# Performance work log

Hardware: AMD Instinct MI355X
Metric: run time of the kernel (lower is better)

The kernel has to match this reference:

```python
import jax, jax.numpy as jnp
import numpy as np

D_MODEL = 1024
IDX_DIM = 64
SEQ = 4096
D_STATE = 64
EXPAND = 1
HEADDIM = 32
D_CONV = 4
D_INNER = EXPAND * D_MODEL
NHEADS = D_INNER // HEADDIM
CONV_DIM = D_INNER + 2 * D_STATE
D_IN_PROJ = 2 * D_INNER + 2 * D_STATE + NHEADS  # z, xBC, dt


def setup_inputs() -> dict:
    key = jax.random.key(0)
    ks = jax.random.split(key, 8)
    def rn(k, shape, scale=1.0):
        return jax.random.normal(k, shape, jnp.float32) * scale
    return {
        "x": rn(ks[0], (SEQ, D_MODEL)),
        "W_in": rn(ks[1], (D_IN_PROJ, D_MODEL), D_MODEL ** -0.5),
        "conv_w": rn(ks[2], (CONV_DIM, D_CONV), D_CONV ** -0.5),
        "conv_b": jnp.zeros((CONV_DIM,), jnp.float32),
        "dt_bias": rn(ks[3], (NHEADS,)),
        "A_log": jnp.log(jnp.arange(1, NHEADS + 1, dtype=jnp.float32)),
        "D": jnp.ones((NHEADS,), jnp.float32),
        "norm_w": jnp.ones((D_INNER,), jnp.float32),
        "W_out": rn(ks[4], (D_MODEL, D_INNER), D_INNER ** -0.5),
        "W_q": rn(ks[5], (IDX_DIM, D_MODEL), D_MODEL ** -0.5),
        "W_k": rn(ks[6], (IDX_DIM, D_MODEL), D_MODEL ** -0.5),
    }


def _silu(v):
    return v * jax.nn.sigmoid(v)


def _mamba2(x, W_in, conv_w, conv_b, dt_bias, A_log, Dp, norm_w, W_out):
    L = x.shape[0]
    zxbcdt = x @ W_in.T  # [L, D_IN_PROJ]
    z, xBC, dt = jnp.split(zxbcdt, [D_INNER, D_INNER + CONV_DIM], axis=-1)
    # depthwise causal conv1d, kernel D_CONV
    xc = jax.lax.conv_general_dilated(
        xBC.T[None],               # [1, C, L]
        conv_w[:, None, :],        # [C, 1, K]
        (1,), [(D_CONV - 1, 0)], feature_group_count=CONV_DIM)[0].T
    xBC = _silu(xc + conv_b)
    xs, B, C = jnp.split(xBC, [D_INNER, D_INNER + D_STATE], axis=-1)
    xs = xs.reshape(L, NHEADS, HEADDIM)
    dt = jax.nn.softplus(dt + dt_bias)   # [L, H]
    A = -jnp.exp(A_log)                  # [H]

    def step(h, inp):
        x_t, B_t, C_t, dt_t = inp        # [H,P], [N], [N], [H]
        dA = jnp.exp(dt_t * A)           # [H]
        h = h * dA[:, None, None] + (dt_t[:, None] * x_t)[:, :, None] * B_t[None, None, :]
        return h, jnp.einsum('hpn,n->hp', h, C_t)

    h0 = jnp.zeros((NHEADS, HEADDIM, D_STATE), x.dtype)
    _, ys = jax.lax.scan(step, h0, (xs, B, C, dt))  # ys: [L, H, P]
    y = ys + Dp[None, :, None] * xs
    y = y.reshape(L, D_INNER)
    y = y * _silu(z)                                 # gated RMSNorm
    y = y * jax.lax.rsqrt(jnp.mean(y * y, axis=-1, keepdims=True) + 1e-5) * norm_w
    return y @ W_out.T


def reference(x, W_in, conv_w, conv_b, dt_bias, A_log, D, norm_w, W_out, W_q, W_k):
    L = x.shape[0]
    x_mamba = _mamba2(x, W_in, conv_w, conv_b, dt_bias, A_log, D, norm_w, W_out)
    q = x_mamba @ W_q.T                  # [L, IDX_DIM]
    k = x @ W_k.T                        # [L, IDX_DIM]
    scores = jnp.einsum('ti,si->ts', q, k) * (IDX_DIM ** -0.5)
    mask = jnp.tril(jnp.ones((L, L), dtype=bool))
    return jnp.where(mask, scores, -jnp.inf)
```

## Files before the change

### kernel.cpp

```cpp
#include <hip/hip_runtime.h>
#include <math.h>

#define L_SEQ 4096
#define DMODEL 1024
#define DINNER 1024
#define DSTATE 64
#define NH 32
#define HD 32
#define CONVD 1152
#define DPROJ2 2272
#define KOFF 2208
#define QC 128
#define NC 32

#define NEG_FILL (-1e30f)

typedef __attribute__((ext_vector_type(8))) short short8;
typedef __attribute__((ext_vector_type(4))) float f32x4;
typedef unsigned short u16;

__device__ __forceinline__ u16 f2bf(float f) {
  unsigned int u = __float_as_uint(f);
  unsigned int r = (u + 0x7fffu + ((u >> 16) & 1u)) >> 16;
  return (u16)r;
}
__device__ __forceinline__ float bf2f(u16 b) {
  unsigned int u = ((unsigned int)b) << 16;
  return __uint_as_float(u);
}
__device__ __forceinline__ short8 pack8(float4 a, float4 b) {
  short8 v;
  v[0] = (short)f2bf(a.x); v[1] = (short)f2bf(a.y);
  v[2] = (short)f2bf(a.z); v[3] = (short)f2bf(a.w);
  v[4] = (short)f2bf(b.x); v[5] = (short)f2bf(b.y);
  v[6] = (short)f2bf(b.z); v[7] = (short)f2bf(b.w);
  return v;
}

__device__ __forceinline__ void g2l16(const void* g, void* l) {
  __builtin_amdgcn_global_load_lds(
      (const __attribute__((address_space(1))) unsigned int*)g,
      (__attribute__((address_space(3))) unsigned int*)l, 16, 0, 0);
}

#define CAST_N0 (L_SEQ * DMODEL / 8)
#define CAST_N1 (2208 * DMODEL / 8)
#define CAST_N2 (64 * DMODEL / 8)
#define CAST_TOTAL (CAST_N0 + CAST_N1 + 2 * CAST_N2)
__global__ __launch_bounds__(256) void cast_all_k(const float* __restrict__ x,
                                                  const float* __restrict__ W_in,
                                                  const float* __restrict__ W_k,
                                                  const float* __restrict__ W_q,
                                                  u16* __restrict__ x_bf,
                                                  u16* __restrict__ Wcat,
                                                  u16* __restrict__ Wq_bf) {
  int gid = blockIdx.x * 256 + threadIdx.x;
  const float* src;
  u16* dst;
  int i;
  if (gid < CAST_N0) { src = x; dst = x_bf; i = gid; }
  else if (gid < CAST_N0 + CAST_N1) { src = W_in; dst = Wcat; i = gid - CAST_N0; }
  else if (gid < CAST_N0 + CAST_N1 + CAST_N2) {
    src = W_k; dst = Wcat + (size_t)2208 * DMODEL; i = gid - CAST_N0 - CAST_N1;
  } else { src = W_q; dst = Wq_bf; i = gid - CAST_N0 - CAST_N1 - CAST_N2; }
  i *= 8;
  float4 f0 = *(const float4*)(src + i);
  float4 f1 = *(const float4*)(src + i + 4);
  *(short8*)(dst + i) = pack8(f0, f1);
}

__global__ __launch_bounds__(256) void transpose_cast_k(const float* __restrict__ in,
                                                        u16* __restrict__ out) {
  __shared__ float tile[64][65];
  int tx = threadIdx.x & 63, ty = threadIdx.x >> 6;
  int bx = blockIdx.x, by = blockIdx.y;
#pragma unroll
  for (int k = 0; k < 16; k++) {
    int r = ty + k * 4;
    tile[r][tx] = in[(size_t)(by * 64 + r) * 1024 + bx * 64 + tx];
  }
  __syncthreads();
#pragma unroll
  for (int k = 0; k < 16; k++) {
    int r = ty + k * 4;
    out[(size_t)(bx * 64 + r) * 1024 + by * 64 + tx] = f2bf(tile[tx][r]);
  }
}

__global__ __launch_bounds__(256) void wqo_k(const u16* __restrict__ Wq,
                                             const u16* __restrict__ WoutT,
                                             u16* __restrict__ Wqo) {
  const int tid = threadIdx.x;
  const int wave = tid >> 6, lane = tid & 63;
  const int l15 = lane & 15, quad = lane >> 4;
  const int j0 = blockIdx.x * 64;
  f32x4 acc[4] = {};
  for (int kk = 0; kk < 32; kk++) {
    short8 b = *(const short8*)(WoutT + (size_t)(j0 + wave * 16 + l15) * 1024 + kk * 32 + quad * 8);
#pragma unroll
    for (int mi = 0; mi < 4; mi++) {
      short8 a = *(const short8*)(Wq + (size_t)(mi * 16 + l15) * 1024 + kk * 32 + quad * 8);
      acc[mi] = __builtin_amdgcn_mfma_f32_16x16x32_bf16(a, b, acc[mi], 0, 0, 0);
    }
  }
#pragma unroll
  for (int mi = 0; mi < 4; mi++)
#pragma unroll
    for (int r = 0; r < 4; r++) {
      int i = mi * 16 + quad * 4 + r;
      Wqo[(size_t)i * 1024 + j0 + wave * 16 + l15] = f2bf(acc[mi][r]);
    }
}

__global__ __launch_bounds__(256) void gemm_n64(const u16* __restrict__ A,
                                                const u16* __restrict__ B,
                                                u16* __restrict__ Cbf,
                                                int M, int N, int K) {
  __shared__ u16 As[128 * 64];
  __shared__ u16 Bs[64 * 64];
  const int tid = threadIdx.x;
  const int wave = tid >> 6, lane = tid & 63;
  const int m0 = blockIdx.x * 128, n0 = blockIdx.y * 64;
  const int wm = (wave >> 1) * 64, wn = (wave & 1) * 32;
  const int l15 = lane & 15, quad = lane >> 4;

  const u16* aptr[4];
  const u16* bptr[2];
  char* ldsA[4];
  char* ldsB[2];
#pragma unroll
  for (int b = 0; b < 4; b++) {
    int ch = b * 256 + tid;
    int row = ch >> 3, q = (ch & 7) ^ (row & 7);
    aptr[b] = A + (size_t)(m0 + row) * K + q * 8;
    ldsA[b] = (char*)As + b * 4096 + wave * 1024;
  }
#pragma unroll
  for (int b = 0; b < 2; b++) {
    int ch = b * 256 + tid;
    int row = ch >> 3, q = (ch & 7) ^ (row & 7);
    int bn = min(n0 + row, N - 1);
    bptr[b] = B + (size_t)bn * K + q * 8;
    ldsB[b] = (char*)Bs + b * 4096 + wave * 1024;
  }

  int offA[2][4], offB[2][2];
#pragma unroll
  for (int kk = 0; kk < 2; kk++) {
#pragma unroll
    for (int i = 0; i < 4; i++) {
      int r = wm + i * 16 + l15;
      offA[kk][i] = r * 64 + ((kk * 4 + quad) ^ (r & 7)) * 8;
    }
#pragma unroll
    for (int j = 0; j < 2; j++) {
      int r = wn + j * 16 + l15;
      offB[kk][j] = r * 64 + ((kk * 4 + quad) ^ (r & 7)) * 8;
    }
  }

  f32x4 acc[4][2] = {};
  for (int k0 = 0; k0 < K; k0 += 64) {
#pragma unroll
    for (int b = 0; b < 4; b++) g2l16(aptr[b] + k0, ldsA[b]);
#pragma unroll
    for (int b = 0; b < 2; b++) g2l16(bptr[b] + k0, ldsB[b]);
    __builtin_amdgcn_s_waitcnt(0);
    __syncthreads();
#pragma unroll
    for (int kk = 0; kk < 2; kk++) {
      short8 af[4], bfr[2];
#pragma unroll
      for (int i = 0; i < 4; i++) af[i] = *(const short8*)(As + offA[kk][i]);
#pragma unroll
      for (int j = 0; j < 2; j++) bfr[j] = *(const short8*)(Bs + offB[kk][j]);
#pragma unroll
      for (int mi = 0; mi < 4; mi++)
#pragma unroll
        for (int ni = 0; ni < 2; ni++)
          acc[mi][ni] = __builtin_amdgcn_mfma_f32_16x16x32_bf16(af[mi], bfr[ni],
                                                                acc[mi][ni], 0, 0, 0);
    }
    __syncthreads();
  }
#pragma unroll
  for (int mi = 0; mi < 4; mi++)
#pragma unroll
    for (int r = 0; r < 4; r++) {
      int grow = m0 + wm + mi * 16 + quad * 4 + r;
#pragma unroll
      for (int ni = 0; ni < 2; ni++) {
        int gcol = n0 + wn + ni * 16 + l15;
        if (gcol < N) Cbf[(size_t)grow * N + gcol] = f2bf(acc[mi][ni][r]);
      }
    }
}

__global__ __launch_bounds__(256) void splitk64(const u16* __restrict__ A,
                                                const u16* __restrict__ B,
                                                float* __restrict__ P,
                                                int M, int K) {
  __shared__ u16 As[128 * 32];
  __shared__ u16 Bs[64 * 32];
  const int tid = threadIdx.x;
  const int wave = tid >> 6, lane = tid & 63;
  const int m0 = blockIdx.x * 128;
  const int ks = blockIdx.y;
  const int wm = (wave >> 1) * 64, wn = (wave & 1) * 32;
  const int l15 = lane & 15, quad = lane >> 4;

  const int c0 = tid, c1 = 256 + tid;
  const int r0 = c0 >> 2, q0 = (c0 & 3) ^ ((r0 >> 1) & 3);
  const int r1 = c1 >> 2, q1 = (c1 & 3) ^ ((r1 >> 1) & 3);
  const int rb = tid >> 2, qb = (tid & 3) ^ ((rb >> 1) & 3);
  const u16* a0 = A + (size_t)(m0 + r0) * K + q0 * 8;
  const u16* a1 = A + (size_t)(m0 + r1) * K + q1 * 8;
  const u16* bptr = B + (size_t)rb * K + qb * 8;
  char* ldsA0 = (char*)As + wave * 1024;
  char* ldsA1 = (char*)As + 4096 + wave * 1024;
  char* ldsB = (char*)Bs + wave * 1024;

  int offA[4], offB[2];
#pragma unroll
  for (int i = 0; i < 4; i++) {
    int ra = wm + i * 16 + l15;
    offA[i] = ra * 32 + (quad ^ ((ra >> 1) & 3)) * 8;
  }
#pragma unroll
  for (int j = 0; j < 2; j++) {
    int rr = wn + j * 16 + l15;
    offB[j] = rr * 32 + (quad ^ ((rr >> 1) & 3)) * 8;
  }

  f32x4 acc[4][2] = {};
  const int kbeg = ks * 128;
  for (int k0 = kbeg; k0 < kbeg + 128; k0 += 32) {
    g2l16(a0 + k0, ldsA0);
    g2l16(a1 + k0, ldsA1);
    g2l16(bptr + k0, ldsB);
    __builtin_amdgcn_s_waitcnt(0);
    __syncthreads();
    short8 af[4], bfr[2];
#pragma unroll
    for (int i = 0; i < 4; i++) af[i] = *(const short8*)(As + offA[i]);
#pragma unroll
    for (int j = 0; j < 2; j++) bfr[j] = *(const short8*)(Bs + offB[j]);
#pragma unroll
    for (int mi = 0; mi < 4; mi++)
#pragma unroll
      for (int ni = 0; ni < 2; ni++)
        acc[mi][ni] = __builtin_amdgcn_mfma_f32_16x16x32_bf16(af[mi], bfr[ni],
                                                              acc[mi][ni], 0, 0, 0);
    __syncthreads();
  }
  float* Pp = P + (size_t)ks * M * 64;
#pragma unroll
  for (int mi = 0; mi < 4; mi++)
#pragma unroll
    for (int r = 0; r < 4; r++) {
      int grow = m0 + wm + mi * 16 + quad * 4 + r;
#pragma unroll
      for (int ni = 0; ni < 2; ni++)
        Pp[(size_t)grow * 64 + wn + ni * 16 + l15] = acc[mi][ni][r];
    }
}

__global__ __launch_bounds__(256) void reduce8_k(const float* __restrict__ P,
                                                 u16* __restrict__ out, int n) {
  int i = blockIdx.x * 256 + threadIdx.x;
  if (i >= n) return;
  float s = 0.f;
#pragma unroll
  for (int ks = 0; ks < 8; ks++) s += P[(size_t)ks * n + i];
  out[i] = f2bf(s);
}

__global__ __launch_bounds__(256) void conv_silu_k(const u16* __restrict__ zx,
                                                   const float* __restrict__ cw,
                                                   const float* __restrict__ cb,
                                                   u16* __restrict__ xbc) {
  int gid = blockIdx.x * 256 + threadIdx.x;
  int t = gid / 144;
  int c0 = (gid - t * 144) * 8;
  float acc[8];
#pragma unroll
  for (int j = 0; j < 8; j++) acc[j] = cb[c0 + j];
  float wv[8][4];
#pragma unroll
  for (int j = 0; j < 8; j++) {
    float4 w4 = *(const float4*)(cw + (c0 + j) * 4);
    wv[j][0] = w4.x; wv[j][1] = w4.y; wv[j][2] = w4.z; wv[j][3] = w4.w;
  }
#pragma unroll
  for (int k = 0; k < 4; k++) {
    int s = t - 3 + k;
    if (s >= 0) {
      short8 v = *(const short8*)(zx + (size_t)s * DPROJ2 + DINNER + c0);
#pragma unroll
      for (int j = 0; j < 8; j++) acc[j] += bf2f((u16)v[j]) * wv[j][k];
    }
  }
  short8 o;
#pragma unroll
  for (int j = 0; j < 8; j++) o[j] = (short)f2bf(acc[j] / (1.f + expf(-acc[j])));
  *(short8*)(xbc + (size_t)t * CONVD + c0) = o;
}

__global__ void dtcum_k(const u16* __restrict__ zx,
                        const float* __restrict__ dt_bias,
                        const float* __restrict__ A_log,
                        float* __restrict__ dtsp,
                        float* __restrict__ aL) {
  int h = blockIdx.x & 31, c = blockIdx.x >> 5;
  int lane = threadIdx.x;
  float negA = -expf(A_log[h]);
  float bias = dt_bias[h];
  float carry = 0.f;
#pragma unroll
  for (int seg = 0; seg < 2; seg++) {
    int t = c * QC + seg * 64 + lane;
    float xv = bf2f(zx[(size_t)t * DPROJ2 + 2176 + h]) + bias;
    float sp = (xv > 20.f) ? xv : log1pf(expf(xv));
    dtsp[(size_t)t * 32 + h] = sp;
    float v = sp * negA;
#pragma unroll
    for (int off = 1; off < 64; off <<= 1) {
      float u = __shfl_up(v, off, 64);
      if (lane >= off) v += u;
    }
    aL[(size_t)t * 32 + h] = carry + v;
    carry += __shfl(v, 63, 64);
  }
}

__global__ __launch_bounds__(256) void chunk_state_mfma(const u16* __restrict__ xbc,
                                                        const float* __restrict__ dtsp,
                                                        const float* __restrict__ aL,
                                                        float* __restrict__ S) {
  int h = blockIdx.x & 31, c = blockIdx.x >> 5;
  int tid = threadIdx.x;
  __shared__ __align__(16) u16 sXs[32 * 136];
  __shared__ __align__(16) u16 sBT[64 * 136];
  __shared__ float scoef[QC];
  if (tid < QC) {
    float aend = aL[(size_t)(c * QC + QC - 1) * 32 + h];
    float a = aL[(size_t)(c * QC + tid) * 32 + h];
    scoef[tid] = expf(aend - a) * dtsp[(size_t)(c * QC + tid) * 32 + h];
  }
  __syncthreads();
  for (int j = tid; j < 32 * QC / 8; j += 256) {
    int s = j & 127, p0 = (j >> 7) * 8;
    short8 v = *(const short8*)(xbc + (size_t)(c * QC + s) * CONVD + h * HD + p0);
    float cf = scoef[s];
#pragma unroll
    for (int e = 0; e < 8; e++) sXs[(p0 + e) * 136 + s] = f2bf(cf * bf2f((u16)v[e]));
  }
  for (int j = tid; j < 64 * QC / 8; j += 256) {
    int s = j & 127, n0 = (j >> 7) * 8;
    short8 v = *(const short8*)(xbc + (size_t)(c * QC + s) * CONVD + DINNER + n0);
#pragma unroll
    for (int e = 0; e < 8; e++) sBT[(n0 + e) * 136 + s] = (u16)v[e];
  }
  __syncthreads();
  const int wave = tid >> 6, lane = tid & 63;
  const int l15 = lane & 15, quad = lane >> 4;
  f32x4 acc[2] = {};
#pragma unroll
  for (int kk = 0; kk < 4; kk++) {
    short8 b = *(const short8*)(sBT + (wave * 16 + l15) * 136 + kk * 32 + quad * 8);
#pragma unroll
    for (int i = 0; i < 2; i++) {
      short8 a = *(const short8*)(sXs + (i * 16 + l15) * 136 + kk * 32 + quad * 8);
      acc[i] = __builtin_amdgcn_mfma_f32_16x16x32_bf16(a, b, acc[i], 0, 0, 0);
    }
  }
  float* Sb = S + ((size_t)c * 32 + h) * 2048;
#pragma unroll
  for (int i = 0; i < 2; i++)
#pragma unroll
    for (int r = 0; r < 4; r++) {
      int p = i * 16 + quad * 4 + r;
      Sb[p * 64 + wave * 16 + l15] = acc[i][r];
    }
}

__global__ __launch_bounds__(256) void state_scan_k(const float* __restrict__ S,
                                                    const float* __restrict__ aL,
                                                    float* __restrict__ Hinit) {
  int idx = blockIdx.x * 256 + threadIdx.x;
  int h = idx >> 11, rem = idx & 2047;
  float E = 0.f;
#pragma unroll
  for (int c = 0; c < NC; c++) {
    size_t o = ((size_t)c * 32 + h) * 2048 + rem;
    Hinit[o] = E;
    float dec = expf(aL[(size_t)(c * QC + QC - 1) * 32 + h]);
    E = E * dec + S[o];
  }
}

__global__ __launch_bounds__(256) void gmat_mfma(const u16* __restrict__ xbc,
                                                 float* __restrict__ G) {
  int c = blockIdx.x;
  int tid = threadIdx.x;
  const int wave = tid >> 6, lane = tid & 63;
  const int wm = (wave >> 1) * 64, wn = (wave & 1) * 64;
  const int l15 = lane & 15, quad = lane >> 4;
  f32x4 acc[4][4] = {};
#pragma unroll
  for (int kk = 0; kk < 2; kk++) {
    short8 a[4], b[4];
#pragma unroll
    for (int i = 0; i < 4; i++) {
      int t = wm + i * 16 + l15;
      a[i] = *(const short8*)(xbc + (size_t)(c * QC + t) * CONVD + DINNER + DSTATE + kk * 32 + quad * 8);
      int s = wn + i * 16 + l15;
      b[i] = *(const short8*)(xbc + (size_t)(c * QC + s) * CONVD + DINNER + kk * 32 + quad * 8);
    }
#pragma unroll
    for (int mi = 0; mi < 4; mi++)
#pragma unroll
      for (int ni = 0; ni < 4; ni++)
        acc[mi][ni] = __builtin_amdgcn_mfma_f32_16x16x32_bf16(a[mi], b[ni],
                                                              acc[mi][ni], 0, 0, 0);
  }
  float* Gb = G + (size_t)c * QC * QC;
#pragma unroll
  for (int mi = 0; mi < 4; mi++)
#pragma unroll
    for (int r = 0; r < 4; r++) {
      int t = wm + mi * 16 + quad * 4 + r;
#pragma unroll
      for (int ni = 0; ni < 4; ni++)
        Gb[(size_t)t * QC + wn + ni * 16 + l15] = acc[mi][ni][r];
    }
}

__global__ __launch_bounds__(256) void yout_mfma(const u16* __restrict__ xbc,
                                                 const float* __restrict__ dtsp,
                                                 const float* __restrict__ aL,
                                                 const float* __restrict__ G,
                                                 const float* __restrict__ Hinit,
                                                 const float* __restrict__ Dv,
                                                 u16* __restrict__ y) {
  int h = blockIdx.x & 31, c = blockIdx.x >> 5;
  int tid = threadIdx.x;
  __shared__ __align__(16) u16 sXT[32 * 136];
  __shared__ float sa[QC];
  __shared__ float sd[QC];

  if (tid < QC) {
    sa[tid] = aL[(size_t)(c * QC + tid) * 32 + h];
    sd[tid] = dtsp[(size_t)(c * QC + tid) * 32 + h];
  }
  for (int j = tid; j < 32 * QC / 8; j += 256) {
    int t = j & 127, p0 = (j >> 7) * 8;
    short8 v = *(const short8*)(xbc + (size_t)(c * QC + t) * CONVD + h * HD + p0);
#pragma unroll
    for (int e = 0; e < 8; e++) sXT[(p0 + e) * 136 + t] = (u16)v[e];
  }
  __syncthreads();

  const int wave = tid >> 6, lane = tid & 63;
  const int l15 = lane & 15, quad = lane >> 4;
  f32x4 acc1[2][2] = {};
  f32x4 acc2[2][2] = {};

#pragma unroll
  for (int kk = 0; kk < 4; kk++) {
    short8 b[2];
#pragma unroll
    for (int j = 0; j < 2; j++)
      b[j] = *(const short8*)(sXT + (j * 16 + l15) * 136 + kk * 32 + quad * 8);
#pragma unroll
    for (int i = 0; i < 2; i++) {
      int rmax = wave * 32 + i * 16 + 15;
      if (kk * 32 > rmax) continue;
      int m = wave * 32 + i * 16 + l15;
      float am = sa[m];
      const float* Gp = G + (size_t)c * QC * QC + (size_t)m * QC + kk * 32 + quad * 8;
      float4 g0 = *(const float4*)Gp;
      float4 g1 = *(const float4*)(Gp + 4);
      float gv[8] = {g0.x, g0.y, g0.z, g0.w, g1.x, g1.y, g1.z, g1.w};
      int s0 = kk * 32 + quad * 8;
      short8 a;
#pragma unroll
      for (int j2 = 0; j2 < 8; j2++) {
        int s = s0 + j2;
        float w = 0.f;
        if (s <= m) w = expf(am - sa[s]) * sd[s] * gv[j2];
        a[j2] = (short)f2bf(w);
      }
#pragma unroll
      for (int j = 0; j < 2; j++)
        acc1[i][j] = __builtin_amdgcn_mfma_f32_16x16x32_bf16(a, b[j], acc1[i][j], 0, 0, 0);
    }
  }

  const float* Hbase = Hinit + ((size_t)c * 32 + h) * 2048;
#pragma unroll
  for (int kk = 0; kk < 2; kk++) {
    short8 b[2];
#pragma unroll
    for (int j = 0; j < 2; j++) {
      const float* Hp = Hbase + (size_t)(j * 16 + l15) * 64 + kk * 32 + quad * 8;
      b[j] = pack8(*(const float4*)Hp, *(const float4*)(Hp + 4));
    }
#pragma unroll
    for (int i = 0; i < 2; i++) {
      int t = wave * 32 + i * 16 + l15;
      short8 a = *(const short8*)(xbc + (size_t)(c * QC + t) * CONVD + DINNER + DSTATE + kk * 32 + quad * 8);
#pragma unroll
      for (int j = 0; j < 2; j++)
        acc2[i][j] = __builtin_amdgcn_mfma_f32_16x16x32_bf16(a, b[j], acc2[i][j], 0, 0, 0);
    }
  }

  float Dh = Dv[h];
#pragma unroll
  for (int i = 0; i < 2; i++) {
#pragma unroll
    for (int r = 0; r < 4; r++) {
      int t = wave * 32 + i * 16 + quad * 4 + r;
      float et = expf(sa[t]);
#pragma unroll
      for (int j = 0; j < 2; j++) {
        int p = j * 16 + l15;
        float xv = bf2f(sXT[p * 136 + t]);
        float val = acc1[i][j][r] + et * acc2[i][j][r] + Dh * xv;
        y[(size_t)(c * QC + t) * DINNER + h * HD + p] = f2bf(val);
      }
    }
  }
}

__global__ __launch_bounds__(256) void rmsnorm_k(const u16* __restrict__ y1,
                                                 const u16* __restrict__ zx,
                                                 const float* __restrict__ nw,
                                                 u16* __restrict__ y2) {
  int t = blockIdx.x, tid = threadIdx.x;
  int d0 = tid * 4;
  ushort4 yv = *(const ushort4*)(y1 + (size_t)t * DINNER + d0);
  ushort4 zv = *(const ushort4*)(zx + (size_t)t * DPROJ2 + d0);
  float v[4];
  float ss = 0.f;
  u16 ya[4] = {yv.x, yv.y, yv.z, yv.w};
  u16 za[4] = {zv.x, zv.y, zv.z, zv.w};
#pragma unroll
  for (int i = 0; i < 4; i++) {
    float z = bf2f(za[i]);
    float val = bf2f(ya[i]) * (z / (1.f + expf(-z)));
    v[i] = val;
    ss += val * val;
  }
#pragma unroll
  for (int off = 32; off > 0; off >>= 1) ss += __shfl_xor(ss, off, 64);
  __shared__ float red[4];
  int wid = tid >> 6, lane = tid & 63;
  if (lane == 0) red[wid] = ss;
  __syncthreads();
  ss = red[0] + red[1] + red[2] + red[3];
  float scale = rsqrtf(ss * (1.f / 1024.f) + 1e-5f);
  float4 w4 = *(const float4*)(nw + d0);
  float wa[4] = {w4.x, w4.y, w4.z, w4.w};
  ushort4 o;
  o.x = f2bf(v[0] * scale * wa[0]);
  o.y = f2bf(v[1] * scale * wa[1]);
  o.z = f2bf(v[2] * scale * wa[2]);
  o.w = f2bf(v[3] * scale * wa[3]);
  *(ushort4*)(y2 + (size_t)t * DINNER + d0) = o;
}

__global__ __launch_bounds__(256) void scores_mfma(const u16* __restrict__ q,
                                                   const u16* __restrict__ kmat,
                                                   int kstride,
                                                   float* __restrict__ out) {
  const int m0 = blockIdx.y * 128, n0 = blockIdx.x * 128;
  const int tid = threadIdx.x;
  if (n0 > m0 + 127) {
    f32x4 f = {NEG_FILL, NEG_FILL, NEG_FILL, NEG_FILL};
    for (int i = tid; i < 128 * 32; i += 256) {
      int row = i >> 5, c4 = (i & 31) << 2;
      __builtin_nontemporal_store(f, (f32x4*)(out + (size_t)(m0 + row) * L_SEQ + n0 + c4));
    }
    return;
  }
  const int wave = tid >> 6, lane = tid & 63;
  const int wm = (wave >> 1) * 64, wn = (wave & 1) * 64;
  const int l15 = lane & 15, quad = lane >> 4;
  f32x4 acc[4][4] = {};
#pragma unroll
  for (int kk = 0; kk < 2; kk++) {
    short8 a[4], b[4];
#pragma unroll
    for (int i = 0; i < 4; i++) {
      a[i] = *(const short8*)(q + (size_t)(m0 + wm + i * 16 + l15) * 64 + kk * 32 + quad * 8);
      b[i] = *(const short8*)(kmat + (size_t)(n0 + wn + i * 16 + l15) * kstride + kk * 32 + quad * 8);
    }
#pragma unroll
    for (int mi = 0; mi < 4; mi++)
#pragma unroll
      for (int ni = 0; ni < 4; ni++)
        acc[mi][ni] = __builtin_amdgcn_mfma_f32_16x16x32_bf16(a[mi], b[ni],
                                                              acc[mi][ni], 0, 0, 0);
  }
#pragma unroll
  for (int mi = 0; mi < 4; mi++)
#pragma unroll
    for (int r = 0; r < 4; r++) {
      int row = m0 + wm + mi * 16 + quad * 4 + r;
#pragma unroll
      for (int ni = 0; ni < 4; ni++) {
        int col = n0 + wn + ni * 16 + l15;
        float val = (col <= row) ? acc[mi][ni][r] * 0.125f : NEG_FILL;
        __builtin_nontemporal_store(val, out + (size_t)row * L_SEQ + col);
      }
    }
}

extern "C" void kernel_launch(void* const* d_in, const int* in_sizes, int n_in,
                              void* d_out, int out_size, void* d_ws, size_t ws_size,
                              hipStream_t stream) {
  const float* x       = (const float*)d_in[0];
  const float* W_in    = (const float*)d_in[1];
  const float* conv_w  = (const float*)d_in[2];
  const float* conv_b  = (const float*)d_in[3];
  const float* dt_bias = (const float*)d_in[4];
  const float* A_log   = (const float*)d_in[5];
  const float* Dv      = (const float*)d_in[6];
  const float* norm_w  = (const float*)d_in[7];
  const float* W_out   = (const float*)d_in[8];
  const float* W_q     = (const float*)d_in[9];
  const float* W_k     = (const float*)d_in[10];
  float* out = (float*)d_out;

  char* ws = (char*)d_ws;
  size_t off = 0;
  auto alloc = [&](size_t bytes) {
    void* p = (void*)(ws + off);
    off += (bytes + 255) & ~(size_t)255;
    return p;
  };
  u16* zx_bf    = (u16*)alloc((size_t)L_SEQ * DPROJ2 * 2);
  u16* xbc_bf   = (u16*)alloc((size_t)L_SEQ * CONVD * 2);
  float* dtsp   = (float*)alloc((size_t)L_SEQ * NH * 4);
  float* aL     = (float*)alloc((size_t)L_SEQ * NH * 4);
  float* S      = (float*)alloc((size_t)NC * NH * HD * DSTATE * 4);
  float* Hinit  = (float*)alloc((size_t)NC * NH * HD * DSTATE * 4);
  float* G      = (float*)alloc((size_t)NC * QC * QC * 4);
  u16* y1_bf    = (u16*)alloc((size_t)L_SEQ * DINNER * 2);
  u16* y2_bf    = (u16*)alloc((size_t)L_SEQ * DINNER * 2);
  u16* x_bf     = (u16*)alloc((size_t)L_SEQ * DMODEL * 2);
  u16* Wcat_bf  = (u16*)alloc((size_t)DPROJ2 * DMODEL * 2);
  u16* WoutT_bf = (u16*)alloc((size_t)DMODEL * DINNER * 2);
  u16* Wq_bf    = (u16*)alloc((size_t)64 * DMODEL * 2);
  u16* Wqo_bf   = (u16*)alloc((size_t)64 * DINNER * 2);
  u16* q_bf     = (u16*)alloc((size_t)L_SEQ * 64 * 2);
  float* Pq = S;

  cast_all_k<<<dim3(CAST_TOTAL / 256), 256, 0, stream>>>(x, W_in, W_k, W_q,
                                                         x_bf, Wcat_bf, Wq_bf);
  transpose_cast_k<<<dim3(16, 16), 256, 0, stream>>>(W_out, WoutT_bf);
  wqo_k<<<dim3(16), 256, 0, stream>>>(Wq_bf, WoutT_bf, Wqo_bf);
  gemm_n64<<<dim3(L_SEQ / 128, (DPROJ2 + 63) / 64), 256, 0, stream>>>(
      x_bf, Wcat_bf, zx_bf, L_SEQ, DPROJ2, DMODEL);
  conv_silu_k<<<dim3(L_SEQ * 144 / 256), 256, 0, stream>>>(zx_bf, conv_w, conv_b, xbc_bf);
  dtcum_k<<<dim3(NC * NH), 64, 0, stream>>>(zx_bf, dt_bias, A_log, dtsp, aL);
  chunk_state_mfma<<<dim3(NC * NH), 256, 0, stream>>>(xbc_bf, dtsp, aL, S);
  state_scan_k<<<dim3(NH * HD * DSTATE / 256), 256, 0, stream>>>(S, aL, Hinit);
  gmat_mfma<<<dim3(NC), 256, 0, stream>>>(xbc_bf, G);
  yout_mfma<<<dim3(NC * NH), 256, 0, stream>>>(xbc_bf, dtsp, aL, G, Hinit, Dv, y1_bf);
  rmsnorm_k<<<dim3(L_SEQ), 256, 0, stream>>>(y1_bf, zx_bf, norm_w, y2_bf);
  splitk64<<<dim3(L_SEQ / 128, 8), 256, 0, stream>>>(y2_bf, Wqo_bf, Pq, L_SEQ, DINNER);
  reduce8_k<<<dim3(L_SEQ * 64 / 256), 256, 0, stream>>>(Pq, q_bf, L_SEQ * 64);
  scores_mfma<<<dim3(32, 32), 256, 0, stream>>>(q_bf, zx_bf + KOFF, DPROJ2, out);
}
```

Before: 248.3 us.

## Merge independent launches and widen input-projection GEMM tile to 128x128

Fuses pairs of independent kernels into single launches by partitioning the block index: cast with W_out transpose, conv with the dt cumsum, and chunk-state with the G matrix. This cuts launch overhead and lets work that was serialized run concurrently. The input-projection GEMM moves from a 128x64 tile with K-step 64 to a 128x128 tile with K-step 32 and a new LDS swizzle, aiming for more MFMA reuse per load. The trade-off is higher register use and wasted work on the padded last N tile.

```diff
diff --git a/kernel.cpp b/kernel.cpp
--- a/kernel.cpp
+++ b/kernel.cpp
@@ -47,43 +47,47 @@
 #define CAST_N1 (2208 * DMODEL / 8)
 #define CAST_N2 (64 * DMODEL / 8)
 #define CAST_TOTAL (CAST_N0 + CAST_N1 + 2 * CAST_N2)
-__global__ __launch_bounds__(256) void cast_all_k(const float* __restrict__ x,
-                                                  const float* __restrict__ W_in,
-                                                  const float* __restrict__ W_k,
-                                                  const float* __restrict__ W_q,
-                                                  u16* __restrict__ x_bf,
-                                                  u16* __restrict__ Wcat,
-                                                  u16* __restrict__ Wq_bf) {
-  int gid = blockIdx.x * 256 + threadIdx.x;
-  const float* src;
-  u16* dst;
-  int i;
-  if (gid < CAST_N0) { src = x; dst = x_bf; i = gid; }
-  else if (gid < CAST_N0 + CAST_N1) { src = W_in; dst = Wcat; i = gid - CAST_N0; }
-  else if (gid < CAST_N0 + CAST_N1 + CAST_N2) {
-    src = W_k; dst = Wcat + (size_t)2208 * DMODEL; i = gid - CAST_N0 - CAST_N1;
-  } else { src = W_q; dst = Wq_bf; i = gid - CAST_N0 - CAST_N1 - CAST_N2; }
-  i *= 8;
-  float4 f0 = *(const float4*)(src + i);
-  float4 f1 = *(const float4*)(src + i + 4);
-  *(short8*)(dst + i) = pack8(f0, f1);
-}
-
-__global__ __launch_bounds__(256) void transpose_cast_k(const float* __restrict__ in,
-                                                        u16* __restrict__ out) {
+#define CAST_BLKS (CAST_TOTAL / 256)
+__global__ __launch_bounds__(256) void cast_tr_k(const float* __restrict__ x,
+                                                 const float* __restrict__ W_in,
+                                                 const float* __restrict__ W_k,
+                                                 const float* __restrict__ W_q,
+                                                 const float* __restrict__ W_out,
+                                                 u16* __restrict__ x_bf,
+                                                 u16* __restrict__ Wcat,
+                                                 u16* __restrict__ Wq_bf,
+                                                 u16* __restrict__ WoutT) {
   __shared__ float tile[64][65];
+  int bid = blockIdx.x;
+  if (bid < CAST_BLKS) {
+    int gid = bid * 256 + threadIdx.x;
+    const float* src;
+    u16* dst;
+    int i;
+    if (gid < CAST_N0) { src = x; dst = x_bf; i = gid; }
+    else if (gid < CAST_N0 + CAST_N1) { src = W_in; dst = Wcat; i = gid - CAST_N0; }
+    else if (gid < CAST_N0 + CAST_N1 + CAST_N2) {
+      src = W_k; dst = Wcat + (size_t)2208 * DMODEL; i = gid - CAST_N0 - CAST_N1;
+    } else { src = W_q; dst = Wq_bf; i = gid - CAST_N0 - CAST_N1 - CAST_N2; }
+    i *= 8;
+    float4 f0 = *(const float4*)(src + i);
+    float4 f1 = *(const float4*)(src + i + 4);
+    *(short8*)(dst + i) = pack8(f0, f1);
+    return;
+  }
+  bid -= CAST_BLKS;
+  int bx = bid & 15, by = bid >> 4;
   int tx = threadIdx.x & 63, ty = threadIdx.x >> 6;
-  int bx = blockIdx.x, by = blockIdx.y;
 #pragma unroll
   for (int k = 0; k < 16; k++) {
     int r = ty + k * 4;
-    tile[r][tx] = in[(size_t)(by * 64 + r) * 1024 + bx * 64 + tx];
+    tile[r][tx] = W_out[(size_t)(by * 64 + r) * 1024 + bx * 64 + tx];
   }
   __syncthreads();
 #pragma unroll
   for (int k = 0; k < 16; k++) {
     int r = ty + k * 4;
-    out[(size_t)(bx * 64 + r) * 1024 + by * 64 + tx] = f2bf(tile[tx][r]);
+    WoutT[(size_t)(bx * 64 + r) * 1024 + by * 64 + tx] = f2bf(tile[tx][r]);
   }
 }
 
@@ -112,75 +116,60 @@
     }
 }
 
-__global__ __launch_bounds__(256) void gemm_n64(const u16* __restrict__ A,
-                                                const u16* __restrict__ B,
-                                                u16* __restrict__ Cbf,
-                                                int M, int N, int K) {
-  __shared__ u16 As[128 * 64];
-  __shared__ u16 Bs[64 * 64];
+__global__ __launch_bounds__(256) void gemm128(const u16* __restrict__ A,
+                                               const u16* __restrict__ B,
+                                               u16* __restrict__ Cbf,
+                                               int M, int N, int K) {
+  __shared__ u16 As[128 * 32];
+  __shared__ u16 Bs[128 * 32];
   const int tid = threadIdx.x;
   const int wave = tid >> 6, lane = tid & 63;
-  const int m0 = blockIdx.x * 128, n0 = blockIdx.y * 64;
-  const int wm = (wave >> 1) * 64, wn = (wave & 1) * 32;
+  const int m0 = blockIdx.x * 128, n0 = blockIdx.y * 128;
+  const int wm = (wave >> 1) * 64, wn = (wave & 1) * 64;
   const int l15 = lane & 15, quad = lane >> 4;
 
-  const u16* aptr[4];
+  const u16* aptr[2];
   const u16* bptr[2];
-  char* ldsA[4];
-  char* ldsB[2];
-#pragma unroll
-  for (int b = 0; b < 4; b++) {
-    int ch = b * 256 + tid;
-    int row = ch >> 3, q = (ch & 7) ^ (row & 7);
-    aptr[b] = A + (size_t)(m0 + row) * K + q * 8;
-    ldsA[b] = (char*)As + b * 4096 + wave * 1024;
-  }
+  char *ldsA[2], *ldsB[2];
 #pragma unroll
   for (int b = 0; b < 2; b++) {
     int ch = b * 256 + tid;
-    int row = ch >> 3, q = (ch & 7) ^ (row & 7);
+    int row = ch >> 2, q = (ch & 3) ^ ((row >> 1) & 3);
+    aptr[b] = A + (size_t)(m0 + row) * K + q * 8;
     int bn = min(n0 + row, N - 1);
     bptr[b] = B + (size_t)bn * K + q * 8;
+    ldsA[b] = (char*)As + b * 4096 + wave * 1024;
     ldsB[b] = (char*)Bs + b * 4096 + wave * 1024;
   }
 
-  int offA[2][4], offB[2][2];
-#pragma unroll
-  for (int kk = 0; kk < 2; kk++) {
-#pragma unroll
-    for (int i = 0; i < 4; i++) {
-      int r = wm + i * 16 + l15;
-      offA[kk][i] = r * 64 + ((kk * 4 + quad) ^ (r & 7)) * 8;
-    }
-#pragma unroll
-    for (int j = 0; j < 2; j++) {
-      int r = wn + j * 16 + l15;
-      offB[kk][j] = r * 64 + ((kk * 4 + quad) ^ (r & 7)) * 8;
-    }
-  }
-
-  f32x4 acc[4][2] = {};
-  for (int k0 = 0; k0 < K; k0 += 64) {
-#pragma unroll
-    for (int b = 0; b < 4; b++) g2l16(aptr[b] + k0, ldsA[b]);
+  int offA[4], offB[4];
+#pragma unroll
+  for (int i = 0; i < 4; i++) {
+    int ra = wm + i * 16 + l15;
+    offA[i] = ra * 32 + (quad ^ ((ra >> 1) & 3)) * 8;
+    int rb = wn + i * 16 + l15;
+    offB[i] = rb * 32 + (quad ^ ((rb >> 1) & 3)) * 8;
+  }
+
+  f32x4 acc[4][4] = {};
+  for (int k0 = 0; k0 < K; k0 += 32) {
+#pragma unroll
+    for (int b = 0; b < 2; b++) g2l16(aptr[b] + k0, ldsA[b]);
 #pragma unroll
     for (int b = 0; b < 2; b++) g2l16(bptr[b] + k0, ldsB[b]);
     __builtin_amdgcn_s_waitcnt(0);
     __syncthreads();
-#pragma unroll
-    for (int kk = 0; kk < 2; kk++) {
-      short8 af[4], bfr[2];
-#pragma unroll
-      for (int i = 0; i < 4; i++) af[i] = *(const short8*)(As + offA[kk][i]);
-#pragma unroll
-      for (int j = 0; j < 2; j++) bfr[j] = *(const short8*)(Bs + offB[kk][j]);
-#pragma unroll
-      for (int mi = 0; mi < 4; mi++)
-#pragma unroll
-        for (int ni = 0; ni < 2; ni++)
-          acc[mi][ni] = __builtin_amdgcn_mfma_f32_16x16x32_bf16(af[mi], bfr[ni],
-                                                                acc[mi][ni], 0, 0, 0);
-    }
+    short8 af[4], bfr[4];
+#pragma unroll
+    for (int i = 0; i < 4; i++) af[i] = *(const short8*)(As + offA[i]);
+#pragma unroll
+    for (int j = 0; j < 4; j++) bfr[j] = *(const short8*)(Bs + offB[j]);
+#pragma unroll
+    for (int mi = 0; mi < 4; mi++)
+#pragma unroll
+      for (int ni = 0; ni < 4; ni++)
+        acc[mi][ni] = __builtin_amdgcn_mfma_f32_16x16x32_bf16(af[mi], bfr[ni],
+                                                              acc[mi][ni], 0, 0, 0);
     __syncthreads();
   }
 #pragma unroll
@@ -189,7 +178,7 @@
     for (int r = 0; r < 4; r++) {
       int grow = m0 + wm + mi * 16 + quad * 4 + r;
 #pragma unroll
-      for (int ni = 0; ni < 2; ni++) {
+      for (int ni = 0; ni < 4; ni++) {
         int gcol = n0 + wn + ni * 16 + l15;
         if (gcol < N) Cbf[(size_t)grow * N + gcol] = f2bf(acc[mi][ni][r]);
       }
@@ -275,44 +264,46 @@
   out[i] = f2bf(s);
 }
 
-__global__ __launch_bounds__(256) void conv_silu_k(const u16* __restrict__ zx,
-                                                   const float* __restrict__ cw,
-                                                   const float* __restrict__ cb,
-                                                   u16* __restrict__ xbc) {
-  int gid = blockIdx.x * 256 + threadIdx.x;
-  int t = gid / 144;
-  int c0 = (gid - t * 144) * 8;
-  float acc[8];
-#pragma unroll
-  for (int j = 0; j < 8; j++) acc[j] = cb[c0 + j];
-  float wv[8][4];
-#pragma unroll
-  for (int j = 0; j < 8; j++) {
-    float4 w4 = *(const float4*)(cw + (c0 + j) * 4);
-    wv[j][0] = w4.x; wv[j][1] = w4.y; wv[j][2] = w4.z; wv[j][3] = w4.w;
-  }
-#pragma unroll
-  for (int k = 0; k < 4; k++) {
-    int s = t - 3 + k;
-    if (s >= 0) {
-      short8 v = *(const short8*)(zx + (size_t)s * DPROJ2 + DINNER + c0);
-#pragma unroll
-      for (int j = 0; j < 8; j++) acc[j] += bf2f((u16)v[j]) * wv[j][k];
-    }
-  }
-  short8 o;
-#pragma unroll
-  for (int j = 0; j < 8; j++) o[j] = (short)f2bf(acc[j] / (1.f + expf(-acc[j])));
-  *(short8*)(xbc + (size_t)t * CONVD + c0) = o;
-}
-
-__global__ void dtcum_k(const u16* __restrict__ zx,
-                        const float* __restrict__ dt_bias,
-                        const float* __restrict__ A_log,
-                        float* __restrict__ dtsp,
-                        float* __restrict__ aL) {
-  int h = blockIdx.x & 31, c = blockIdx.x >> 5;
-  int lane = threadIdx.x;
+#define CONV_BLKS (L_SEQ * 144 / 256)
+__global__ __launch_bounds__(256) void conv_dt_k(const u16* __restrict__ zx,
+                                                 const float* __restrict__ cw,
+                                                 const float* __restrict__ cb,
+                                                 u16* __restrict__ xbc,
+                                                 const float* __restrict__ dt_bias,
+                                                 const float* __restrict__ A_log,
+                                                 float* __restrict__ dtsp,
+                                                 float* __restrict__ aL) {
+  if (blockIdx.x < CONV_BLKS) {
+    int gid = blockIdx.x * 256 + threadIdx.x;
+    int t = gid / 144;
+    int c0 = (gid - t * 144) * 8;
+    float acc[8];
+#pragma unroll
+    for (int j = 0; j < 8; j++) acc[j] = cb[c0 + j];
+    float wv[8][4];
+#pragma unroll
+    for (int j = 0; j < 8; j++) {
+      float4 w4 = *(const float4*)(cw + (c0 + j) * 4);
+      wv[j][0] = w4.x; wv[j][1] = w4.y; wv[j][2] = w4.z; wv[j][3] = w4.w;
+    }
+#pragma unroll
+    for (int k = 0; k < 4; k++) {
+      int s = t - 3 + k;
+      if (s >= 0) {
+        short8 v = *(const short8*)(zx + (size_t)s * DPROJ2 + DINNER + c0);
+#pragma unroll
+        for (int j = 0; j < 8; j++) acc[j] += bf2f((u16)v[j]) * wv[j][k];
+      }
+    }
+    short8 o;
+#pragma unroll
+    for (int j = 0; j < 8; j++) o[j] = (short)f2bf(acc[j] / (1.f + expf(-acc[j])));
+    *(short8*)(xbc + (size_t)t * CONVD + c0) = o;
+    return;
+  }
+  int w = threadIdx.x >> 6, lane = threadIdx.x & 63;
+  int idx = (blockIdx.x - CONV_BLKS) * 4 + w;
+  int h = idx & 31, c = idx >> 5;
   float negA = -expf(A_log[h]);
   float bias = dt_bias[h];
   float carry = 0.f;
@@ -333,54 +324,88 @@
   }
 }
 
-__global__ __launch_bounds__(256) void chunk_state_mfma(const u16* __restrict__ xbc,
-                                                        const float* __restrict__ dtsp,
-                                                        const float* __restrict__ aL,
-                                                        float* __restrict__ S) {
-  int h = blockIdx.x & 31, c = blockIdx.x >> 5;
+__global__ __launch_bounds__(256) void csg_k(const u16* __restrict__ xbc,
+                                             const float* __restrict__ dtsp,
+                                             const float* __restrict__ aL,
+                                             float* __restrict__ S,
+                                             float* __restrict__ G) {
   int tid = threadIdx.x;
+  const int wave = tid >> 6, lane = tid & 63;
+  const int l15 = lane & 15, quad = lane >> 4;
   __shared__ __align__(16) u16 sXs[32 * 136];
   __shared__ __align__(16) u16 sBT[64 * 136];
   __shared__ float scoef[QC];
-  if (tid < QC) {
-    float aend = aL[(size_t)(c * QC + QC - 1) * 32 + h];
-    float a = aL[(size_t)(c * QC + tid) * 32 + h];
-    scoef[tid] = expf(aend - a) * dtsp[(size_t)(c * QC + tid) * 32 + h];
-  }
-  __syncthreads();
-  for (int j = tid; j < 32 * QC / 8; j += 256) {
-    int s = j & 127, p0 = (j >> 7) * 8;
-    short8 v = *(const short8*)(xbc + (size_t)(c * QC + s) * CONVD + h * HD + p0);
-    float cf = scoef[s];
-#pragma unroll
-    for (int e = 0; e < 8; e++) sXs[(p0 + e) * 136 + s] = f2bf(cf * bf2f((u16)v[e]));
-  }
-  for (int j = tid; j < 64 * QC / 8; j += 256) {
-    int s = j & 127, n0 = (j >> 7) * 8;
-    short8 v = *(const short8*)(xbc + (size_t)(c * QC + s) * CONVD + DINNER + n0);
-#pragma unroll
-    for (int e = 0; e < 8; e++) sBT[(n0 + e) * 136 + s] = (u16)v[e];
-  }
-  __syncthreads();
-  const int wave = tid >> 6, lane = tid & 63;
-  const int l15 = lane & 15, quad = lane >> 4;
-  f32x4 acc[2] = {};
-#pragma unroll
-  for (int kk = 0; kk < 4; kk++) {
-    short8 b = *(const short8*)(sBT + (wave * 16 + l15) * 136 + kk * 32 + quad * 8);
-#pragma unroll
-    for (int i = 0; i < 2; i++) {
-      short8 a = *(const short8*)(sXs + (i * 16 + l15) * 136 + kk * 32 + quad * 8);
-      acc[i] = __builtin_amdgcn_mfma_f32_16x16x32_bf16(a, b, acc[i], 0, 0, 0);
-    }
-  }
-  float* Sb = S + ((size_t)c * 32 + h) * 2048;
-#pragma unroll
-  for (int i = 0; i < 2; i++)
+  if (blockIdx.x < (unsigned)(NC * NH)) {
+    int h = blockIdx.x & 31, c = blockIdx.x >> 5;
+    if (tid < QC) {
+      float aend = aL[(size_t)(c * QC + QC - 1) * 32 + h];
+      float a = aL[(size_t)(c * QC + tid) * 32 + h];
+      scoef[tid] = expf(aend - a) * dtsp[(size_t)(c * QC + tid) * 32 + h];
+    }
+    __syncthreads();
+    for (int j = tid; j < 32 * QC / 8; j += 256) {
+      int s = j & 127, p0 = (j >> 7) * 8;
+      short8 v = *(const short8*)(xbc + (size_t)(c * QC + s) * CONVD + h * HD + p0);
+      float cf = scoef[s];
+#pragma unroll
+      for (int e = 0; e < 8; e++) sXs[(p0 + e) * 136 + s] = f2bf(cf * bf2f((u16)v[e]));
+    }
+    for (int j = tid; j < 64 * QC / 8; j += 256) {
+      int s = j & 127, n0 = (j >> 7) * 8;
+      short8 v = *(const short8*)(xbc + (size_t)(c * QC + s) * CONVD + DINNER + n0);
+#pragma unroll
+      for (int e = 0; e < 8; e++) sBT[(n0 + e) * 136 + s] = (u16)v[e];
+    }
+    __syncthreads();
+    f32x4 acc[2] = {};
+#pragma unroll
+    for (int kk = 0; kk < 4; kk++) {
+      short8 b = *(const short8*)(sBT + (wave * 16 + l15) * 136 + kk * 32 + quad * 8);
+#pragma unroll
+      for (int i = 0; i < 2; i++) {
+        short8 a = *(const short8*)(sXs + (i * 16 + l15) * 136 + kk * 32 + quad * 8);
+        acc[i] = __builtin_amdgcn_mfma_f32_16x16x32_bf16(a, b, acc[i], 0, 0, 0);
+      }
+    }
+    float* Sb = S + ((size_t)c * 32 + h) * 2048;
+#pragma unroll
+    for (int i = 0; i < 2; i++)
+#pragma unroll
+      for (int r = 0; r < 4; r++) {
+        int p = i * 16 + quad * 4 + r;
+        Sb[p * 64 + wave * 16 + l15] = acc[i][r];
+      }
+    return;
+  }
+  int c = blockIdx.x - NC * NH;
+  const int wm = (wave >> 1) * 64, wn = (wave & 1) * 64;
+  f32x4 acc[4][4] = {};
+#pragma unroll
+  for (int kk = 0; kk < 2; kk++) {
+    short8 a[4], b[4];
+#pragma unroll
+    for (int i = 0; i < 4; i++) {
+      int t = wm + i * 16 + l15;
+      a[i] = *(const short8*)(xbc + (size_t)(c * QC + t) * CONVD + DINNER + DSTATE + kk * 32 + quad * 8);
+      int s = wn + i * 16 + l15;
+      b[i] = *(const short8*)(xbc + (size_t)(c * QC + s) * CONVD + DINNER + kk * 32 + quad * 8);
+    }
+#pragma unroll
+    for (int mi = 0; mi < 4; mi++)
+#pragma unroll
+      for (int ni = 0; ni < 4; ni++)
+        acc[mi][ni] = __builtin_amdgcn_mfma_f32_16x16x32_bf16(a[mi], b[ni],
+                                                              acc[mi][ni], 0, 0, 0);
+  }
+  float* Gb = G + (size_t)c * QC * QC;
+#pragma unroll
+  for (int mi = 0; mi < 4; mi++)
 #pragma unroll
     for (int r = 0; r < 4; r++) {
-      int p = i * 16 + quad * 4 + r;
-      Sb[p * 64 + wave * 16 + l15] = acc[i][r];
+      int t = wm + mi * 16 + quad * 4 + r;
+#pragma unroll
+      for (int ni = 0; ni < 4; ni++)
+        Gb[(size_t)t * QC + wn + ni * 16 + l15] = acc[mi][ni][r];
     }
 }
 
@@ -397,43 +422,6 @@
     float dec = expf(aL[(size_t)(c * QC + QC - 1) * 32 + h]);
     E = E * dec + S[o];
   }
-}
-
-__global__ __launch_bounds__(256) void gmat_mfma(const u16* __restrict__ xbc,
-                                                 float* __restrict__ G) {
-  int c = blockIdx.x;
-  int tid = threadIdx.x;
-  const int wave = tid >> 6, lane = tid & 63;
-  const int wm = (wave >> 1) * 64, wn = (wave & 1) * 64;
-  const int l15 = lane & 15, quad = lane >> 4;
-  f32x4 acc[4][4] = {};
-#pragma unroll
-  for (int kk = 0; kk < 2; kk++) {
-    short8 a[4], b[4];
-#pragma unroll
-    for (int i = 0; i < 4; i++) {
-      int t = wm + i * 16 + l15;
-      a[i] = *(const short8*)(xbc + (size_t)(c * QC + t) * CONVD + DINNER + DSTATE + kk * 32 + quad * 8);
-      int s = wn + i * 16 + l15;
-      b[i] = *(const short8*)(xbc + (size_t)(c * QC + s) * CONVD + DINNER + kk * 32 + quad * 8);
-    }
-#pragma unroll
-    for (int mi = 0; mi < 4; mi++)
-#pragma unroll
-      for (int ni = 0; ni < 4; ni++)
-        acc[mi][ni] = __builtin_amdgcn_mfma_f32_16x16x32_bf16(a[mi], b[ni],
-                                                              acc[mi][ni], 0, 0, 0);
-  }
-  float* Gb = G + (size_t)c * QC * QC;
-#pragma unroll
-  for (int mi = 0; mi < 4; mi++)
-#pragma unroll
-    for (int r = 0; r < 4; r++) {
-      int t = wm + mi * 16 + quad * 4 + r;
-#pragma unroll
-      for (int ni = 0; ni < 4; ni++)
-        Gb[(size_t)t * QC + wn + ni * 16 + l15] = acc[mi][ni][r];
-    }
 }
 
 __global__ __launch_bounds__(256) void yout_mfma(const u16* __restrict__ xbc,
@@ -658,17 +646,15 @@
   u16* q_bf     = (u16*)alloc((size_t)L_SEQ * 64 * 2);
   float* Pq = S;
 
-  cast_all_k<<<dim3(CAST_TOTAL / 256), 256, 0, stream>>>(x, W_in, W_k, W_q,
-                                                         x_bf, Wcat_bf, Wq_bf);
-  transpose_cast_k<<<dim3(16, 16), 256, 0, stream>>>(W_out, WoutT_bf);
+  cast_tr_k<<<dim3(CAST_BLKS + 256), 256, 0, stream>>>(x, W_in, W_k, W_q, W_out,
+                                                       x_bf, Wcat_bf, Wq_bf, WoutT_bf);
   wqo_k<<<dim3(16), 256, 0, stream>>>(Wq_bf, WoutT_bf, Wqo_bf);
-  gemm_n64<<<dim3(L_SEQ / 128, (DPROJ2 + 63) / 64), 256, 0, stream>>>(
+  gemm128<<<dim3(L_SEQ / 128, (DPROJ2 + 127) / 128), 256, 0, stream>>>(
       x_bf, Wcat_bf, zx_bf, L_SEQ, DPROJ2, DMODEL);
-  conv_silu_k<<<dim3(L_SEQ * 144 / 256), 256, 0, stream>>>(zx_bf, conv_w, conv_b, xbc_bf);
-  dtcum_k<<<dim3(NC * NH), 64, 0, stream>>>(zx_bf, dt_bias, A_log, dtsp, aL);
-  chunk_state_mfma<<<dim3(NC * NH), 256, 0, stream>>>(xbc_bf, dtsp, aL, S);
+  conv_dt_k<<<dim3(CONV_BLKS + NC * NH / 4), 256, 0, stream>>>(
+      zx_bf, conv_w, conv_b, xbc_bf, dt_bias, A_log, dtsp, aL);
+  csg_k<<<dim3(NC * NH + NC), 256, 0, stream>>>(xbc_bf, dtsp, aL, S, G);
   state_scan_k<<<dim3(NH * HD * DSTATE / 256), 256, 0, stream>>>(S, aL, Hinit);
-  gmat_mfma<<<dim3(NC), 256, 0, stream>>>(xbc_bf, G);
   yout_mfma<<<dim3(NC * NH), 256, 0, stream>>>(xbc_bf, dtsp, aL, G, Hinit, Dv, y1_bf);
   rmsnorm_k<<<dim3(L_SEQ), 256, 0, stream>>>(y1_bf, zx_bf, norm_w, y2_bf);
   splitk64<<<dim3(L_SEQ / 128, 8), 256, 0, stream>>>(y2_bf, Wqo_bf, Pq, L_SEQ, DINNER);
```

After: 246.0 us. No clear change (-0.9%).
